# Kernel tuning notes

Measured on AMD Instinct MI355X. Metric: run time of the kernel, lower is better.

The kernel has to match this reference:

```python
import jax, jax.numpy as jnp
import numpy as np

B, T, D, E = 8, 2048, 256, 4
D_E = D // E


def setup_inputs() -> dict:
    key = jax.random.key(0)
    ks = jax.random.split(key, 12)
    s = 1.0 / np.sqrt(D)
    x = jax.random.normal(ks[0], (B, T, D), dtype=jnp.float32)
    # ensure max(seq_len) == T so the padded input matches this_batch_padlen
    seq_len = jnp.concatenate([
        jax.random.randint(ks[1], (B - 1,), T // 2, T),
        jnp.array([T]),
    ]).astype(jnp.int32)
    return {
        "x": x,
        "seq_len": seq_len,
        "wq": jax.random.uniform(ks[2], (D, D), jnp.float32, -s, s),
        "bq": jax.random.uniform(ks[3], (D,), jnp.float32, -s, s),
        "wk": jax.random.uniform(ks[4], (D, D), jnp.float32, -s, s),
        "bk": jax.random.uniform(ks[5], (D,), jnp.float32, -s, s),
        "wv": jax.random.uniform(ks[6], (D, D), jnp.float32, -s, s),
        "bv": jax.random.uniform(ks[7], (D,), jnp.float32, -s, s),
        "wo": jax.random.uniform(ks[8], (D, D), jnp.float32, -s, s),
        "bo": jax.random.uniform(ks[9], (D,), jnp.float32, -s, s),
        "theta": jnp.array([50.0], dtype=jnp.float32),
    }


def _split_heads(y):
    # faithful to torch: [B,T,D] -> permute(0,2,1) -> [B,D,T] -> reshape(B*E, T, D_E)
    return jnp.transpose(y, (0, 2, 1)).reshape(B * E, T, D_E)


def reference(x, seq_len, wq, bq, wk, bk, wv, bv, wo, bo, theta):
    Q = _split_heads(x @ wq.T + bq)          # [B*E, T, D_E]
    K = _split_heads(x @ wk.T + bk)          # [B*E, T, D_E]
    V = _split_heads(x @ wv.T + bv)          # [B*E, T, D_E]

    # padding mask: zero out query rows (and key cols) past seq_len[i]
    pos = jnp.arange(T)
    valid = (pos[None, :] < seq_len[:, None])                 # [B, T]
    mask_q = jnp.repeat(valid, E, axis=0).astype(Q.dtype)     # [B*E, T]
    Q = Q * mask_q[:, :, None]
    K = K * mask_q[:, :, None]

    scale = jnp.sqrt(jnp.float32(T))
    att = jnp.einsum('bqd,bkd->bqk', Q, K) / scale            # [B*E, T, T]

    # Gaussian positional penalty (is_punish=True)
    tpos = jnp.arange(T, dtype=jnp.float32)
    diff = tpos[None, :] - tpos[:, None]                      # j - i
    punish = jnp.exp(-(diff ** 2) / (theta[0] ** 2))          # [T, T]
    att = att * punish[None, :, :]

    att = jnp.where(att == 0.0, jnp.float32(-2e20), att)
    att = jax.nn.softmax(att, axis=2)

    ctx = jnp.einsum('bqk,bkd->bqd', att, V)                  # [B*E, T, D_E]
    # faithful inverse of _split_heads: permute(0,2,1)->reshape(B,D,T)->permute
    ctx = jnp.transpose(jnp.transpose(ctx, (0, 2, 1)).reshape(B, D, T), (0, 2, 1))
    A = ctx @ wo.T + bo
    return A + x
```

## Files before the change

kernel.cpp:

```cpp
#include <hip/hip_runtime.h>
#include <math.h>
#include <stdint.h>

#define B_SZ   8
#define T_SEQ  2048
#define DIM    256
#define NH     32
#define DE     64
#define BAND   509
#define THR_N  641
#define M_ROWS (B_SZ * T_SEQ)

typedef __attribute__((ext_vector_type(8))) short short8;
typedef __attribute__((ext_vector_type(4))) float floatx4;
typedef unsigned short ushort_t;

__device__ __forceinline__ ushort_t f2bf(float x) {
    unsigned u = __float_as_uint(x);
    u += 0x7fffu + ((u >> 16) & 1u);
    return (ushort_t)(u >> 16);
}
__device__ __forceinline__ float bf2f(ushort_t b) {
    return __uint_as_float(((unsigned)b) << 16);
}
__device__ __forceinline__ unsigned pack2(float a, float b) {
    return (unsigned)f2bf(a) | ((unsigned)f2bf(b) << 16);
}

__global__ __launch_bounds__(256) void prep_kernel(
    const float* __restrict__ x,
    const float* __restrict__ wq, const float* __restrict__ wk,
    const float* __restrict__ wv, const float* __restrict__ wo,
    const float* __restrict__ theta,
    ushort_t* __restrict__ xb, ushort_t* __restrict__ wb,
    float* __restrict__ thr_g, float* __restrict__ pdf_g)
{
    const int bid = blockIdx.x, tid = threadIdx.x;
    if (bid < 2048) {
        size_t i8 = ((size_t)bid * 256 + tid) * 8;
        float4 a = *(const float4*)(x + i8);
        float4 b = *(const float4*)(x + i8 + 4);
        uint4 o;
        o.x = pack2(a.x, a.y); o.y = pack2(a.z, a.w);
        o.z = pack2(b.x, b.y); o.w = pack2(b.z, b.w);
        *(uint4*)(xb + i8) = o;
    } else if (bid < 2176) {
        size_t w8 = ((size_t)(bid - 2048) * 256 + tid) * 8;
        int which = (int)(w8 >> 16);
        const float* src = (which == 0) ? wq : (which == 1) ? wk : (which == 2) ? wv : wo;
        size_t off = w8 & 65535;
        float4 a = *(const float4*)(src + off);
        float4 b = *(const float4*)(src + off + 4);
        uint4 o;
        o.x = pack2(a.x, a.y); o.y = pack2(a.z, a.w);
        o.z = pack2(b.x, b.y); o.w = pack2(b.z, b.w);
        *(uint4*)(wb + w8) = o;
    } else {
        int i = (bid - 2176) * 256 + tid;
        if (i >= THR_N) return;
        float df  = (float)i;
        float th  = theta[0];
        float arg = (-(df * df)) / (th * th);
        double pdd = exp((double)arg);
        double outv;
        if (pdd < 1.17549435082228751e-38) {
            outv = rint(pdd * 0x1p149) * 0x1p-149;
        } else {
            outv = (double)(float)pdd;
        }
        thr_g[i] = (outv == 0.0) ? __builtin_inff() : (float)(0x1p-150 / outv);
        pdf_g[i] = (float)outv;
    }
}

__global__ __launch_bounds__(256, 2) void proj_qkv_mfma(
    const ushort_t* __restrict__ xb, const ushort_t* __restrict__ wb,
    const float* __restrict__ bq, const float* __restrict__ bk,
    const float* __restrict__ bv, const int* __restrict__ seq_len,
    ushort_t* __restrict__ Qh, ushort_t* __restrict__ Kh, ushort_t* __restrict__ Vh)
{
    const int wave = threadIdx.x >> 6, lane = threadIdx.x & 63;
    const int quad = lane >> 4, l15 = lane & 15;
    const int task = blockIdx.x * 4 + wave;
    const int nt64 = task % 12;
    const int mstrip = task / 12;
    const int mode = nt64 >> 2;
    const int nloc_base = (nt64 & 3) * 64;
    const ushort_t* Wp = wb + (size_t)mode * 65536;
    const int m0 = mstrip * 64;
    const int bb = m0 >> 11;
    const int th0 = (m0 >> 6) & 31;
    const int sl = seq_len[bb];
    ushort_t* outp = (mode == 0) ? Qh : (mode == 1) ? Kh : Vh;
    const float* bias = (mode == 0) ? bq : (mode == 1) ? bk : bv;
    const int hh = bb * 4 + (nloc_base >> 6);
    const float oscale = (mode == 0) ? 0.022097086912079612f : 1.0f;

    short8 Bf[4][8];
    #pragma unroll
    for (int nt = 0; nt < 4; ++nt) {
        int nrow = nloc_base + nt * 16 + l15;
        #pragma unroll
        for (int ks = 0; ks < 8; ++ks)
            Bf[nt][ks] = *(const short8*)(Wp + (size_t)nrow * 256 + ks * 32 + quad * 8);
    }
    float bias4[4]; int qv[4];
    #pragma unroll
    for (int nt = 0; nt < 4; ++nt) {
        int dl = nloc_base + nt * 16 + l15;
        bias4[nt] = bias[dl];
        qv[nt] = (dl & 63) * 32 + th0;
    }

    short8 Acur[8];
    #pragma unroll
    for (int ks = 0; ks < 8; ++ks)
        Acur[ks] = *(const short8*)(xb + (size_t)(m0 + l15) * 256 + ks * 32 + quad * 8);

    #pragma unroll
    for (int mb = 0; mb < 4; ++mb) {
        const int mb0 = m0 + mb * 16;
        short8 Anext[8];
        if (mb < 3) {
            #pragma unroll
            for (int ks = 0; ks < 8; ++ks)
                Anext[ks] = *(const short8*)(xb + (size_t)(mb0 + 16 + l15) * 256 + ks * 32 + quad * 8);
        }
        floatx4 acc[4];
        #pragma unroll
        for (int nt = 0; nt < 4; ++nt) acc[nt] = (floatx4){0.f, 0.f, 0.f, 0.f};
        #pragma unroll
        for (int ks = 0; ks < 8; ++ks)
            #pragma unroll
            for (int nt = 0; nt < 4; ++nt)
                acc[nt] = __builtin_amdgcn_mfma_f32_16x16x32_bf16(Acur[ks], Bf[nt][ks], acc[nt], 0, 0, 0);
        const int e_base = (mb0 & 63) + quad * 4;
        #pragma unroll
        for (int nt = 0; nt < 4; ++nt) {
            bool msk = (mode <= 1) && (qv[nt] >= sl);
            float v0 = msk ? 0.f : (acc[nt][0] + bias4[nt]) * oscale;
            float v1 = msk ? 0.f : (acc[nt][1] + bias4[nt]) * oscale;
            float v2 = msk ? 0.f : (acc[nt][2] + bias4[nt]) * oscale;
            float v3 = msk ? 0.f : (acc[nt][3] + bias4[nt]) * oscale;
            uint2 pk; pk.x = pack2(v0, v1); pk.y = pack2(v2, v3);
            *(uint2*)(outp + (((size_t)hh * T_SEQ + qv[nt]) << 6) + e_base) = pk;
        }
        #pragma unroll
        for (int ks = 0; ks < 8; ++ks) Acur[ks] = Anext[ks];
    }
}

__global__ __launch_bounds__(256) void meanv_partial(const ushort_t* __restrict__ Vh,
                                                     float* __restrict__ mv) {
    __shared__ float red[32][72];
    const int blk = blockIdx.x;
    const int h = blk >> 3, chunk = blk & 7;
    const int tid = threadIdx.x;
    const int r0 = tid >> 3;
    const int es = (tid & 7) * 8;
    const ushort_t* p = Vh + ((size_t)h * T_SEQ + chunk * 256 + r0) * DE + es;
    float s[8] = {};
    #pragma unroll
    for (int k = 0; k < 8; ++k) {
        uint4 u = *(const uint4*)(p + (size_t)k * 32 * DE);
        const ushort_t* w = (const ushort_t*)&u;
        #pragma unroll
        for (int i = 0; i < 8; ++i) s[i] += bf2f(w[i]);
    }
    #pragma unroll
    for (int i = 0; i < 8; ++i) red[r0][es + i] = s[i];
    __syncthreads();
    if (tid < 64) {
        float t = 0.f;
        #pragma unroll
        for (int g = 0; g < 32; ++g) t += red[g][tid];
        atomicAdd(&mv[h * DE + tid], t);
    }
}

__global__ __launch_bounds__(256) void attn_mfma_kernel(
    const ushort_t* __restrict__ Qh, const ushort_t* __restrict__ Kh,
    const ushort_t* __restrict__ Vh, const float* __restrict__ thr_g,
    const float* __restrict__ pdf_g, const float* __restrict__ meanv,
    const int* __restrict__ seq_len, ushort_t* __restrict__ ctxb)
{
    __shared__ ushort_t Ks [64][72];
    __shared__ ushort_t VTs[64][72];
    __shared__ ushort_t Ps [4][16][72];
    __shared__ float pdfs[384];
    __shared__ float thrs[320];

    const int tid  = threadIdx.x;
    const int wave = tid >> 6;
    const int lane = tid & 63;
    const int quad = lane >> 4;
    const int l15  = lane & 15;
    const int bid   = blockIdx.x;
    const int inner = bid >> 3;
    const int h  = ((inner >> 5) << 3) | (bid & 7);
    const int q0 = (inner & 31) * 64;
    const int b  = h >> 2;
    const int sl = seq_len[b];
    const float invT = 1.0f / (float)T_SEQ;
    ushort_t* outbase = ctxb + ((size_t)b * T_SEQ + q0) * DIM + (size_t)(h & 3) * 64;

    if (q0 >= sl) {
        #pragma unroll
        for (int nt = 0; nt < 4; ++nt) {
            ushort_t mval = f2bf(meanv[h * DE + l15 + 16 * nt] * invT);
            #pragma unroll
            for (int r = 0; r < 4; ++r) {
                int row = wave * 16 + quad * 4 + r;
                outbase[(size_t)row * DIM + l15 + 16 * nt] = mval;
            }
        }
        return;
    }

    for (int i = tid; i < 384; i += 256) pdfs[i] = pdf_g[i];
    for (int i = tid; i < 320; i += 256) thrs[i] = thr_g[321 + i];

    short8 qa0, qa1;
    {
        const ushort_t* qp = Qh + ((size_t)h * T_SEQ + q0 + wave * 16 + l15) * DE + quad * 8;
        qa0 = *(const short8*)(qp);
        qa1 = *(const short8*)(qp + 32);
    }

    float l_acc[4] = {0.f, 0.f, 0.f, 0.f};
    floatx4 cacc[4];
    #pragma unroll
    for (int nt = 0; nt < 4; ++nt) cacc[nt] = (floatx4){0.f, 0.f, 0.f, 0.f};

    int jlo = q0 - BAND;      if (jlo < 0) jlo = 0;
    int jhi = q0 + 63 + BAND; if (jhi > sl - 1) jhi = sl - 1;
    const int jt0 = jlo >> 6, jt1 = jhi >> 6;

    const int krow = tid >> 3;
    const int kc8  = (tid & 7) * 8;
    uint4 kpre0, kpre1, vpre0, vpre1;
    {
        const ushort_t* ksrc = Kh + ((size_t)h * T_SEQ + (jt0 << 6)) * DE;
        const ushort_t* vsrc = Vh + ((size_t)h * T_SEQ + (jt0 << 6)) * DE;
        kpre0 = *(const uint4*)(ksrc + (size_t)krow * DE + kc8);
        kpre1 = *(const uint4*)(ksrc + (size_t)(krow + 32) * DE + kc8);
        vpre0 = *(const uint4*)(vsrc + (size_t)lane * DE + wave * 16);
        vpre1 = *(const uint4*)(vsrc + (size_t)lane * DE + wave * 16 + 8);
    }

    for (int jt = jt0; jt <= jt1; ++jt) {
        const int j0 = jt << 6;
        __syncthreads();
        *(uint4*)&Ks[krow][kc8]      = kpre0;
        *(uint4*)&Ks[krow + 32][kc8] = kpre1;
        {
            union { uint4 u4[2]; ushort_t us[16]; } vv;
            vv.u4[0] = vpre0; vv.u4[1] = vpre1;
            #pragma unroll
            for (int k = 0; k < 16; ++k) VTs[wave * 16 + k][lane] = vv.us[k];
        }
        __syncthreads();
        if (jt < jt1) {
            const ushort_t* ksrc = Kh + ((size_t)h * T_SEQ + j0 + 64) * DE;
            const ushort_t* vsrc = Vh + ((size_t)h * T_SEQ + j0 + 64) * DE;
            kpre0 = *(const uint4*)(ksrc + (size_t)krow * DE + kc8);
            kpre1 = *(const uint4*)(ksrc + (size_t)(krow + 32) * DE + kc8);
            vpre0 = *(const uint4*)(vsrc + (size_t)lane * DE + wave * 16);
            vpre1 = *(const uint4*)(vsrc + (size_t)lane * DE + wave * 16 + 8);
        }

        floatx4 S[4];
        #pragma unroll
        for (int nt = 0; nt < 4; ++nt) {
            short8 kb0 = *(const short8*)&Ks[l15 + 16 * nt][quad * 8];
            short8 kb1 = *(const short8*)&Ks[l15 + 16 * nt][32 + quad * 8];
            floatx4 z = {0.f, 0.f, 0.f, 0.f};
            z = __builtin_amdgcn_mfma_f32_16x16x32_bf16(qa0, kb0, z, 0, 0, 0);
            z = __builtin_amdgcn_mfma_f32_16x16x32_bf16(qa1, kb1, z, 0, 0, 0);
            S[nt] = z;
        }

        const int off = j0 - q0;
        float p[4][4];
        if (off >= -320 && off <= 320) {
            #pragma unroll
            for (int nt = 0; nt < 4; ++nt) {
                int jg = j0 + l15 + 16 * nt;
                bool jv = (jg < sl);
                #pragma unroll
                for (int r = 0; r < 4; ++r) {
                    int qg = q0 + wave * 16 + quad * 4 + r;
                    float pd = pdfs[abs(jg - qg)];
                    float av = S[nt][r] * pd;
                    av = jv ? av : -1e30f;
                    p[nt][r] = __expf(av);
                }
            }
        } else {
            #pragma unroll
            for (int nt = 0; nt < 4; ++nt) {
                int jg = j0 + l15 + 16 * nt;
                #pragma unroll
                for (int r = 0; r < 4; ++r) {
                    int qg = q0 + wave * 16 + quad * 4 + r;
                    float t = thrs[abs(jg - qg) - 321];
                    p[nt][r] = (fabsf(S[nt][r]) > t) ? 1.0f : 0.0f;
                }
            }
        }

        #pragma unroll
        for (int nt = 0; nt < 4; ++nt)
            #pragma unroll
            for (int r = 0; r < 4; ++r) {
                l_acc[r] += p[nt][r];
                Ps[wave][quad * 4 + r][l15 + 16 * nt] = f2bf(p[nt][r]);
            }

        short8 pa0 = *(const short8*)&Ps[wave][l15][quad * 8];
        short8 pa1 = *(const short8*)&Ps[wave][l15][32 + quad * 8];
        #pragma unroll
        for (int nt = 0; nt < 4; ++nt) {
            short8 vb0 = *(const short8*)&VTs[l15 + 16 * nt][quad * 8];
            short8 vb1 = *(const short8*)&VTs[l15 + 16 * nt][32 + quad * 8];
            floatx4 c = cacc[nt];
            c = __builtin_amdgcn_mfma_f32_16x16x32_bf16(pa0, vb0, c, 0, 0, 0);
            c = __builtin_amdgcn_mfma_f32_16x16x32_bf16(pa1, vb1, c, 0, 0, 0);
            cacc[nt] = c;
        }
    }

    #pragma unroll
    for (int r = 0; r < 4; ++r) {
        float lv = l_acc[r];
        #pragma unroll
        for (int o = 1; o <= 8; o <<= 1) lv += __shfl_xor(lv, o);
        l_acc[r] = 1.0f / lv;
    }
    #pragma unroll
    for (int nt = 0; nt < 4; ++nt) {
        #pragma unroll
        for (int r = 0; r < 4; ++r) {
            int row = wave * 16 + quad * 4 + r;
            int qg = q0 + row;
            float o = cacc[nt][r] * l_acc[r];
            if (qg >= sl) o = meanv[h * DE + l15 + 16 * nt] * invT;
            outbase[(size_t)row * DIM + l15 + 16 * nt] = f2bf(o);
        }
    }
}

__global__ __launch_bounds__(256, 2) void proj_o_mfma(
    const ushort_t* __restrict__ ctx, const ushort_t* __restrict__ wb,
    const float* __restrict__ bo, const float* __restrict__ x,
    float* __restrict__ out)
{
    const int wave = threadIdx.x >> 6, lane = threadIdx.x & 63;
    const int quad = lane >> 4, l15 = lane & 15;
    const int task = blockIdx.x * 4 + wave;
    const int nt64 = task & 3;
    const int mstrip = task >> 2;
    const int n0 = nt64 * 64;
    const ushort_t* Wp = wb + (size_t)3 * 65536;
    const int m0 = mstrip * 64;

    short8 Bf[4][8];
    #pragma unroll
    for (int nt = 0; nt < 4; ++nt) {
        int nrow = n0 + nt * 16 + l15;
        #pragma unroll
        for (int ks = 0; ks < 8; ++ks)
            Bf[nt][ks] = *(const short8*)(Wp + (size_t)nrow * 256 + ks * 32 + quad * 8);
    }
    float bias4[4];
    #pragma unroll
    for (int nt = 0; nt < 4; ++nt) bias4[nt] = bo[n0 + nt * 16 + l15];

    short8 Acur[8];
    #pragma unroll
    for (int ks = 0; ks < 8; ++ks)
        Acur[ks] = *(const short8*)(ctx + (size_t)(m0 + l15) * 256 + ks * 32 + quad * 8);

    #pragma unroll
    for (int mb = 0; mb < 4; ++mb) {
        const int mb0 = m0 + mb * 16;
        short8 Anext[8];
        if (mb < 3) {
            #pragma unroll
            for (int ks = 0; ks < 8; ++ks)
                Anext[ks] = *(const short8*)(ctx + (size_t)(mb0 + 16 + l15) * 256 + ks * 32 + quad * 8);
        }
        floatx4 acc[4];
        #pragma unroll
        for (int nt = 0; nt < 4; ++nt) acc[nt] = (floatx4){0.f, 0.f, 0.f, 0.f};
        #pragma unroll
        for (int ks = 0; ks < 8; ++ks)
            #pragma unroll
            for (int nt = 0; nt < 4; ++nt)
                acc[nt] = __builtin_amdgcn_mfma_f32_16x16x32_bf16(Acur[ks], Bf[nt][ks], acc[nt], 0, 0, 0);
        #pragma unroll
        for (int nt = 0; nt < 4; ++nt) {
            int d = n0 + nt * 16 + l15;
            #pragma unroll
            for (int r = 0; r < 4; ++r) {
                size_t mi = (size_t)(mb0 + quad * 4 + r) * 256 + d;
                out[mi] = acc[nt][r] + bias4[nt] + x[mi];
            }
        }
        #pragma unroll
        for (int ks = 0; ks < 8; ++ks) Acur[ks] = Anext[ks];
    }
}

extern "C" void kernel_launch(void* const* d_in, const int* in_sizes, int n_in,
                              void* d_out, int out_size, void* d_ws, size_t ws_size,
                              hipStream_t stream)
{
    (void)in_sizes; (void)n_in; (void)out_size; (void)ws_size;
    const float* x  = (const float*)d_in[0];
    const int*   sl = (const int*)d_in[1];
    const float* wq = (const float*)d_in[2];
    const float* bq = (const float*)d_in[3];
    const float* wk = (const float*)d_in[4];
    const float* bk = (const float*)d_in[5];
    const float* wv = (const float*)d_in[6];
    const float* bv = (const float*)d_in[7];
    const float* wo = (const float*)d_in[8];
    const float* bo = (const float*)d_in[9];
    const float* th = (const float*)d_in[10];
    float* out = (float*)d_out;

    char* ws = (char*)d_ws;
    const size_t SZH = (size_t)M_ROWS * DIM * sizeof(ushort_t);
    ushort_t* xb  = (ushort_t*)(ws);
    ushort_t* wb  = (ushort_t*)(ws + SZH);
    ushort_t* Qh  = (ushort_t*)(ws + SZH + 524288);
    ushort_t* Kh  = (ushort_t*)(ws + 2*SZH + 524288);
    ushort_t* Vh  = (ushort_t*)(ws + 3*SZH + 524288);
    ushort_t* Cb  = (ushort_t*)(ws + 4*SZH + 524288);
    float*    Mv  = (float*)   (ws + 5*SZH + 524288);
    float*    Thr = (float*)   (ws + 5*SZH + 524288 + 8192);
    float*    Pdf = (float*)   (ws + 5*SZH + 524288 + 12288);

    hipMemsetAsync(Mv, 0, NH * DE * sizeof(float), stream);
    prep_kernel<<<dim3(2179), dim3(256), 0, stream>>>(x, wq, wk, wv, wo, th, xb, wb, Thr, Pdf);
    proj_qkv_mfma<<<dim3(768), dim3(256), 0, stream>>>(xb, wb, bq, bk, bv, sl, Qh, Kh, Vh);
    meanv_partial<<<dim3(256), dim3(256), 0, stream>>>(Vh, Mv);
    attn_mfma_kernel<<<dim3(T_SEQ/64 * NH), dim3(256), 0, stream>>>(Qh, Kh, Vh, Thr, Pdf, Mv, sl, Cb);
    proj_o_mfma<<<dim3(256), dim3(256), 0, stream>>>(Cb, wb, bo, x, out);
}
```

Baseline: 191.0 us.

## Pre-transpose V globally, stage QKV stores through LDS, pack P writes

Adds a vtrans_kernel that writes V in a [head][e][t] layout. The attention kernel can then fill its V^T shared tile with vector stores instead of 16 scalar transposed LDS writes per tile. The QKV projection now stages its output tile in shared memory so global writes are coalesced per row, and P is packed into 64-bit LDS stores. The extra kernel launch and V round-trip through global memory are the main added costs.

Result: faster. 186.6 us (-2.3%).

```diff
diff --git a/kernel.cpp b/kernel.cpp
--- a/kernel.cpp
+++ b/kernel.cpp
@@ -8,7 +8,6 @@
 #define NH     32
 #define DE     64
 #define BAND   509
-#define THR_N  641
 #define M_ROWS (B_SZ * T_SEQ)
 
 typedef __attribute__((ext_vector_type(8))) short short8;
@@ -25,6 +24,15 @@
 }
 __device__ __forceinline__ unsigned pack2(float a, float b) {
     return (unsigned)f2bf(a) | ((unsigned)f2bf(b) << 16);
+}
+
+__device__ __forceinline__ double pd_exact(int d, float th) {
+    float df  = (float)d;
+    float arg = (-(df * df)) / (th * th);
+    double pdd = exp((double)arg);
+    if (pdd < 1.17549435082228751e-38)
+        return rint(pdd * 0x1p149) * 0x1p-149;
+    return (double)(float)pdd;
 }
 
 __global__ __launch_bounds__(256) void prep_kernel(
@@ -57,19 +65,12 @@
         *(uint4*)(wb + w8) = o;
     } else {
         int i = (bid - 2176) * 256 + tid;
-        if (i >= THR_N) return;
-        float df  = (float)i;
-        float th  = theta[0];
-        float arg = (-(df * df)) / (th * th);
-        double pdd = exp((double)arg);
-        double outv;
-        if (pdd < 1.17549435082228751e-38) {
-            outv = rint(pdd * 0x1p149) * 0x1p-149;
-        } else {
-            outv = (double)(float)pdd;
-        }
-        thr_g[i] = (outv == 0.0) ? __builtin_inff() : (float)(0x1p-150 / outv);
-        pdf_g[i] = (float)outv;
+        float th = theta[0];
+        if (i < 384) pdf_g[i] = (float)pd_exact(i, th);
+        if (i < 288) {
+            double pdv = pd_exact(321 + i, th);
+            thr_g[i] = (pdv == 0.0) ? __builtin_inff() : (float)(0x1p-150 / pdv);
+        }
     }
 }
 
@@ -79,6 +80,7 @@
     const float* __restrict__ bv, const int* __restrict__ seq_len,
     ushort_t* __restrict__ Qh, ushort_t* __restrict__ Kh, ushort_t* __restrict__ Vh)
 {
+    __shared__ __align__(16) ushort_t Ls[4][64][68];
     const int wave = threadIdx.x >> 6, lane = threadIdx.x & 63;
     const int quad = lane >> 4, l15 = lane & 15;
     const int task = blockIdx.x * 4 + wave;
@@ -104,13 +106,9 @@
         for (int ks = 0; ks < 8; ++ks)
             Bf[nt][ks] = *(const short8*)(Wp + (size_t)nrow * 256 + ks * 32 + quad * 8);
     }
-    float bias4[4]; int qv[4];
-    #pragma unroll
-    for (int nt = 0; nt < 4; ++nt) {
-        int dl = nloc_base + nt * 16 + l15;
-        bias4[nt] = bias[dl];
-        qv[nt] = (dl & 63) * 32 + th0;
-    }
+    float bias4[4];
+    #pragma unroll
+    for (int nt = 0; nt < 4; ++nt) bias4[nt] = bias[nloc_base + nt * 16 + l15];
 
     short8 Acur[8];
     #pragma unroll
@@ -134,19 +132,61 @@
             #pragma unroll
             for (int nt = 0; nt < 4; ++nt)
                 acc[nt] = __builtin_amdgcn_mfma_f32_16x16x32_bf16(Acur[ks], Bf[nt][ks], acc[nt], 0, 0, 0);
-        const int e_base = (mb0 & 63) + quad * 4;
         #pragma unroll
         for (int nt = 0; nt < 4; ++nt) {
-            bool msk = (mode <= 1) && (qv[nt] >= sl);
-            float v0 = msk ? 0.f : (acc[nt][0] + bias4[nt]) * oscale;
-            float v1 = msk ? 0.f : (acc[nt][1] + bias4[nt]) * oscale;
-            float v2 = msk ? 0.f : (acc[nt][2] + bias4[nt]) * oscale;
-            float v3 = msk ? 0.f : (acc[nt][3] + bias4[nt]) * oscale;
+            float v0 = (acc[nt][0] + bias4[nt]) * oscale;
+            float v1 = (acc[nt][1] + bias4[nt]) * oscale;
+            float v2 = (acc[nt][2] + bias4[nt]) * oscale;
+            float v3 = (acc[nt][3] + bias4[nt]) * oscale;
             uint2 pk; pk.x = pack2(v0, v1); pk.y = pack2(v2, v3);
-            *(uint2*)(outp + (((size_t)hh * T_SEQ + qv[nt]) << 6) + e_base) = pk;
+            *(uint2*)&Ls[wave][nt * 16 + l15][mb * 16 + quad * 4] = pk;
         }
         #pragma unroll
         for (int ks = 0; ks < 8; ++ks) Acur[ks] = Anext[ks];
+    }
+
+    #pragma unroll
+    for (int s = 0; s < 16; ++s) {
+        int dl = s * 4 + quad;
+        int e0 = l15 * 4;
+        uint2 pk = *(const uint2*)&Ls[wave][dl][e0];
+        int q = dl * 32 + th0;
+        if (mode <= 1 && q >= sl) { pk.x = 0u; pk.y = 0u; }
+        *(uint2*)(outp + (((size_t)hh * T_SEQ + q) << 6) + e0) = pk;
+    }
+}
+
+__global__ __launch_bounds__(256) void vtrans_kernel(const ushort_t* __restrict__ Vh,
+                                                     ushort_t* __restrict__ VTp)
+{
+    __shared__ ushort_t Vs[256][66];
+    const int tid = threadIdx.x;
+    const int h = blockIdx.x >> 3, chunk = blockIdx.x & 7;
+    const ushort_t* src = Vh + ((size_t)(h * T_SEQ + chunk * 256)) * DE;
+    #pragma unroll
+    for (int rep = 0; rep < 8; ++rep) {
+        int f = rep * 256 + tid;
+        int row = f >> 3, c8 = (f & 7) * 8;
+        *(uint4*)&Vs[row][c8] = *(const uint4*)(src + (size_t)row * DE + c8);
+    }
+    __syncthreads();
+    const int w = tid >> 6, lane = tid & 63;
+    const int half = lane >> 5;
+    const int c32 = lane & 31;
+    const int cbase = c32 * 8;
+    const int blk = cbase >> 6;
+    const int cin = cbase & 63;
+    #pragma unroll
+    for (int rr = 0; rr < 8; ++rr) {
+        int e = w * 16 + rr * 2 + half;
+        ushort_t tmp[8];
+        #pragma unroll
+        for (int t = 0; t < 8; ++t) {
+            int ci = cin + t;
+            int j = blk * 64 + (ci >> 2) + 16 * (ci & 3);
+            tmp[t] = Vs[j][e];
+        }
+        *(uint4*)(VTp + ((size_t)(h * DE + e)) * T_SEQ + chunk * 256 + cbase) = *(uint4*)tmp;
     }
 }
 
@@ -180,15 +220,15 @@
 
 __global__ __launch_bounds__(256) void attn_mfma_kernel(
     const ushort_t* __restrict__ Qh, const ushort_t* __restrict__ Kh,
-    const ushort_t* __restrict__ Vh, const float* __restrict__ thr_g,
-    const float* __restrict__ pdf_g, const float* __restrict__ meanv,
+    const ushort_t* __restrict__ VTp, const float* __restrict__ thr_g,
+    const float* __restrict__ pdf_g, const float* __restrict__ mvs,
     const int* __restrict__ seq_len, ushort_t* __restrict__ ctxb)
 {
     __shared__ ushort_t Ks [64][72];
     __shared__ ushort_t VTs[64][72];
     __shared__ ushort_t Ps [4][16][72];
     __shared__ float pdfs[384];
-    __shared__ float thrs[320];
+    __shared__ float thrs[288];
 
     const int tid  = threadIdx.x;
     const int wave = tid >> 6;
@@ -207,18 +247,16 @@
     if (q0 >= sl) {
         #pragma unroll
         for (int nt = 0; nt < 4; ++nt) {
-            ushort_t mval = f2bf(meanv[h * DE + l15 + 16 * nt] * invT);
-            #pragma unroll
-            for (int r = 0; r < 4; ++r) {
-                int row = wave * 16 + quad * 4 + r;
-                outbase[(size_t)row * DIM + l15 + 16 * nt] = mval;
-            }
+            ushort_t mval = f2bf(mvs[h * DE + l15 + 16 * nt] * invT);
+            #pragma unroll
+            for (int r = 0; r < 4; ++r)
+                outbase[(size_t)(wave * 16 + quad * 4 + r) * DIM + l15 + 16 * nt] = mval;
         }
         return;
     }
 
     for (int i = tid; i < 384; i += 256) pdfs[i] = pdf_g[i];
-    for (int i = tid; i < 320; i += 256) thrs[i] = thr_g[321 + i];
+    for (int i = tid; i < 288; i += 256) thrs[i] = thr_g[i];
 
     short8 qa0, qa1;
     {
@@ -238,35 +276,31 @@
 
     const int krow = tid >> 3;
     const int kc8  = (tid & 7) * 8;
+    const ushort_t* Kbp = Kh + (size_t)h * T_SEQ * DE;
+    const ushort_t* Vbp = VTp + (size_t)h * DE * T_SEQ;
     uint4 kpre0, kpre1, vpre0, vpre1;
     {
-        const ushort_t* ksrc = Kh + ((size_t)h * T_SEQ + (jt0 << 6)) * DE;
-        const ushort_t* vsrc = Vh + ((size_t)h * T_SEQ + (jt0 << 6)) * DE;
-        kpre0 = *(const uint4*)(ksrc + (size_t)krow * DE + kc8);
-        kpre1 = *(const uint4*)(ksrc + (size_t)(krow + 32) * DE + kc8);
-        vpre0 = *(const uint4*)(vsrc + (size_t)lane * DE + wave * 16);
-        vpre1 = *(const uint4*)(vsrc + (size_t)lane * DE + wave * 16 + 8);
+        const int j0 = jt0 << 6;
+        kpre0 = *(const uint4*)(Kbp + (size_t)(j0 + krow) * DE + kc8);
+        kpre1 = *(const uint4*)(Kbp + (size_t)(j0 + krow + 32) * DE + kc8);
+        vpre0 = *(const uint4*)(Vbp + (size_t)krow * T_SEQ + j0 + kc8);
+        vpre1 = *(const uint4*)(Vbp + (size_t)(krow + 32) * T_SEQ + j0 + kc8);
     }
 
     for (int jt = jt0; jt <= jt1; ++jt) {
         const int j0 = jt << 6;
         __syncthreads();
-        *(uint4*)&Ks[krow][kc8]      = kpre0;
-        *(uint4*)&Ks[krow + 32][kc8] = kpre1;
-        {
-            union { uint4 u4[2]; ushort_t us[16]; } vv;
-            vv.u4[0] = vpre0; vv.u4[1] = vpre1;
-            #pragma unroll
-            for (int k = 0; k < 16; ++k) VTs[wave * 16 + k][lane] = vv.us[k];
-        }
+        *(uint4*)&Ks[krow][kc8]       = kpre0;
+        *(uint4*)&Ks[krow + 32][kc8]  = kpre1;
+        *(uint4*)&VTs[krow][kc8]      = vpre0;
+        *(uint4*)&VTs[krow + 32][kc8] = vpre1;
         __syncthreads();
         if (jt < jt1) {
-            const ushort_t* ksrc = Kh + ((size_t)h * T_SEQ + j0 + 64) * DE;
-            const ushort_t* vsrc = Vh + ((size_t)h * T_SEQ + j0 + 64) * DE;
-            kpre0 = *(const uint4*)(ksrc + (size_t)krow * DE + kc8);
-            kpre1 = *(const uint4*)(ksrc + (size_t)(krow + 32) * DE + kc8);
-            vpre0 = *(const uint4*)(vsrc + (size_t)lane * DE + wave * 16);
-            vpre1 = *(const uint4*)(vsrc + (size_t)lane * DE + wave * 16 + 8);
+            const int jn = j0 + 64;
+            kpre0 = *(const uint4*)(Kbp + (size_t)(jn + krow) * DE + kc8);
+            kpre1 = *(const uint4*)(Kbp + (size_t)(jn + krow + 32) * DE + kc8);
+            vpre0 = *(const uint4*)(Vbp + (size_t)krow * T_SEQ + jn + kc8);
+            vpre1 = *(const uint4*)(Vbp + (size_t)(krow + 32) * T_SEQ + jn + kc8);
         }
 
         floatx4 S[4];
@@ -289,9 +323,9 @@
                 bool jv = (jg < sl);
                 #pragma unroll
                 for (int r = 0; r < 4; ++r) {
-                    int qg = q0 + wave * 16 + quad * 4 + r;
-                    float pd = pdfs[abs(jg - qg)];
-                    float av = S[nt][r] * pd;
+                    int dd = jg - (q0 + wave * 16 + quad * 4 + r);
+                    dd = dd < 0 ? -dd : dd;
+                    float av = S[nt][r] * pdfs[dd];
                     av = jv ? av : -1e30f;
                     p[nt][r] = __expf(av);
                 }
@@ -302,21 +336,21 @@
                 int jg = j0 + l15 + 16 * nt;
                 #pragma unroll
                 for (int r = 0; r < 4; ++r) {
-                    int qg = q0 + wave * 16 + quad * 4 + r;
-                    float t = thrs[abs(jg - qg) - 321];
-                    p[nt][r] = (fabsf(S[nt][r]) > t) ? 1.0f : 0.0f;
+                    int dd = jg - (q0 + wave * 16 + quad * 4 + r);
+                    dd = dd < 0 ? -dd : dd;
+                    p[nt][r] = (fabsf(S[nt][r]) > thrs[dd - 321]) ? 1.0f : 0.0f;
                 }
             }
         }
 
         #pragma unroll
-        for (int nt = 0; nt < 4; ++nt)
-            #pragma unroll
-            for (int r = 0; r < 4; ++r) {
-                l_acc[r] += p[nt][r];
-                Ps[wave][quad * 4 + r][l15 + 16 * nt] = f2bf(p[nt][r]);
-            }
-
+        for (int r = 0; r < 4; ++r) {
+            l_acc[r] += (p[0][r] + p[1][r]) + (p[2][r] + p[3][r]);
+            uint2 pk;
+            pk.x = pack2(p[0][r], p[1][r]);
+            pk.y = pack2(p[2][r], p[3][r]);
+            *(uint2*)&Ps[wave][quad * 4 + r][l15 * 4] = pk;
+        }
         short8 pa0 = *(const short8*)&Ps[wave][l15][quad * 8];
         short8 pa1 = *(const short8*)&Ps[wave][l15][32 + quad * 8];
         #pragma unroll
@@ -344,7 +378,7 @@
             int row = wave * 16 + quad * 4 + r;
             int qg = q0 + row;
             float o = cacc[nt][r] * l_acc[r];
-            if (qg >= sl) o = meanv[h * DE + l15 + 16 * nt] * invT;
+            if (qg >= sl) o = mvs[h * DE + l15 + 16 * nt] * invT;
             outbase[(size_t)row * DIM + l15 + 16 * nt] = f2bf(o);
         }
     }
@@ -437,15 +471,17 @@
     ushort_t* Qh  = (ushort_t*)(ws + SZH + 524288);
     ushort_t* Kh  = (ushort_t*)(ws + 2*SZH + 524288);
     ushort_t* Vh  = (ushort_t*)(ws + 3*SZH + 524288);
-    ushort_t* Cb  = (ushort_t*)(ws + 4*SZH + 524288);
-    float*    Mv  = (float*)   (ws + 5*SZH + 524288);
-    float*    Thr = (float*)   (ws + 5*SZH + 524288 + 8192);
-    float*    Pdf = (float*)   (ws + 5*SZH + 524288 + 12288);
+    ushort_t* VTp = (ushort_t*)(ws + 4*SZH + 524288);
+    ushort_t* Cb  = (ushort_t*)(ws + 5*SZH + 524288);
+    float*    Mv  = (float*)   (ws + 6*SZH + 524288);
+    float*    Thr = (float*)   (ws + 6*SZH + 524288 + 8192);
+    float*    Pdf = (float*)   (ws + 6*SZH + 524288 + 12288);
 
     hipMemsetAsync(Mv, 0, NH * DE * sizeof(float), stream);
-    prep_kernel<<<dim3(2179), dim3(256), 0, stream>>>(x, wq, wk, wv, wo, th, xb, wb, Thr, Pdf);
+    prep_kernel<<<dim3(2178), dim3(256), 0, stream>>>(x, wq, wk, wv, wo, th, xb, wb, Thr, Pdf);
     proj_qkv_mfma<<<dim3(768), dim3(256), 0, stream>>>(xb, wb, bq, bk, bv, sl, Qh, Kh, Vh);
+    vtrans_kernel<<<dim3(NH * 8), dim3(256), 0, stream>>>(Vh, VTp);
     meanv_partial<<<dim3(256), dim3(256), 0, stream>>>(Vh, Mv);
-    attn_mfma_kernel<<<dim3(T_SEQ/64 * NH), dim3(256), 0, stream>>>(Qh, Kh, Vh, Thr, Pdf, Mv, sl, Cb);
+    attn_mfma_kernel<<<dim3(1024), dim3(256), 0, stream>>>(Qh, Kh, VTp, Thr, Pdf, Mv, sl, Cb);
     proj_o_mfma<<<dim3(256), dim3(256), 0, stream>>>(Cb, wb, bo, x, out);
 }
```
